# Kernel tuning notes

Hardware: AMD Instinct MI355X
Metric: run time of the kernel (lower is better)

## Reference

```python
import jax, jax.numpy as jnp
import numpy as np

N_WAY = 5
MAX_PER_CLASS = 256
SIGMA_GRID = np.array([0.5, 1.0, 2.0, 4.0], dtype=np.float32)
NUM_NEG = 1
GAMMA = 0.1
HARD_POOL = 8
MEDIAN_K = 512
EPS = 1e-12
LAMBDA_MMD = 0.1


def _pairwise_sq(x, y=None):
    # squared euclidean distances between rows of x [n,d] and y [m,d]
    if y is None:
        y = x
    x2 = jnp.sum(x * x, axis=1, keepdims=True)
    y2 = jnp.sum(y * y, axis=1, keepdims=True).T
    return jnp.maximum(x2 + y2 - 2.0 * (x @ y.T), 0.0)


def _row_norm(x):
    return x / (jnp.linalg.norm(x, axis=1, keepdims=True) + EPS)


def _rbf_multi(d, sigmas):
    # multi-bandwidth RBF kernel sum: sum_s exp(-d / (2 s^2))
    return jnp.sum(jnp.exp(-d[None] / (2.0 * sigmas[:, None, None] ** 2)), axis=0)


def _mmd2(Da, Db, Dab, sigmas):
    # biased MMD^2 estimator (unbiased=False)
    m = (_rbf_multi(Da, sigmas).mean() + _rbf_multi(Db, sigmas).mean()
         - 2.0 * _rbf_multi(Dab, sigmas).mean())
    return jnp.maximum(m, 0.0)


def _median_sigmas(xa, xb):
    # median-heuristic bandwidth (no grad); concat has <= MEDIAN_K rows by construction
    z = jnp.concatenate([xa, xb], axis=0)
    d = _pairwise_sq(z)
    ds = jnp.sort(d.ravel())
    n = ds.shape[0]
    nz = jnp.sum(d <= 0)  # number of zero entries (diag + exact dups)
    idx = jnp.minimum(nz + (n - nz - 1) // 2, n - 1)  # lower median of positive entries
    med = jnp.take(ds, idx)
    base = jnp.where(nz >= n, jnp.asarray(1.0, z.dtype), jnp.sqrt(med + 1e-6))
    return jax.lax.stop_gradient(base) * jnp.asarray(SIGMA_GRID, z.dtype)


def _gather_indices(l_s, l_q):
    # host-side ragged per-class index extraction + deterministic subsample
    ls = np.asarray(l_s)
    lq = np.asarray(l_q)
    sup, ns, qry, nq = {}, {}, {}, {}
    for c in range(1, N_WAY + 1):
        idx = np.nonzero(ls[c - 1] == 1)[0]
        if idx.size >= 2:
            ns[c] = int(idx.size)
            if idx.size > MAX_PER_CLASS:
                rng = np.random.default_rng(1000 + c)
                idx = idx[rng.permutation(idx.size)[:MAX_PER_CLASS]]
            sup[c] = idx
        m, nn = np.nonzero(lq == c)
        if m.size >= 2:
            nq[c] = int(m.size)
            if m.size > MAX_PER_CLASS:
                rng = np.random.default_rng(2000 + c)
                pick = rng.permutation(m.size)[:MAX_PER_CLASS]
                m, nn = m[pick], nn[pick]
            qry[c] = (m, nn)
    return sup, ns, qry, nq


def _class_feats(f_s, f_q, sup, qry):
    # gather per-class rows and L2-normalize them
    fq = jnp.transpose(f_q, (0, 2, 1))  # [M_B, Nb, C]
    xas = {c: _row_norm(f_s[c - 1].T[idx]) for c, idx in sup.items()}
    xbs = {c: _row_norm(fq[m, nn]) for c, (m, nn) in qry.items()}
    return xas, xbs


def _select_picks(f_s, f_q, sup, qry):
    # hard-negative selection on concrete values (detached in the original)
    xas, xbs = _class_feats(f_s, f_q, sup, qry)
    picks = {}
    for c in sorted(set(xas) & set(xbs)):
        xb = xbs[c]
        Db = _pairwise_sq(xb)
        sig_pos = _median_sigmas(xas[c], xb)
        neg = [k for k in xas if k != c]
        if NUM_NEG == 0 or not neg:
            picks[c] = []
            continue
        scr = [(float(_mmd2(_pairwise_sq(xas[k]), Db, _pairwise_sq(xas[k], xb), sig_pos)), k) for k in neg]
        scr.sort(key=lambda t: t[0])
        pool = [k for _, k in scr[:max(HARD_POOL, NUM_NEG)]]
        ex = [(float(_mmd2(_pairwise_sq(xas[k]), Db, _pairwise_sq(xas[k], xb), _median_sigmas(xas[k], xb))), k) for k in pool]
        ex.sort(key=lambda t: t[0])
        picks[c] = [k for _, k in ex[:NUM_NEG]]
    return picks


def _loss(f_s, f_q, sup, ns, qry, nq, picks):
    xas, xbs = _class_feats(f_s, f_q, sup, qry)
    total = jnp.zeros((), f_s.dtype)
    valid_w = jnp.zeros((), f_s.dtype)
    for c in sorted(set(xas) & set(xbs)):
        xa, xb = xas[c], xbs[c]
        Db = _pairwise_sq(xb)
        sig_pos = _median_sigmas(xa, xb)
        mmd_pos = _mmd2(_pairwise_sq(xa), Db, _pairwise_sq(xa, xb), sig_pos)
        negs = []
        for k in picks.get(c, []):
            xk = xas[k]
            sig_k = _median_sigmas(xk, xb)
            negs.append(_mmd2(_pairwise_sq(xk), Db, _pairwise_sq(xk, xb), sig_k))
        if negs:
            mmd_neg = jnp.stack(negs).mean()
            loss_c = jax.nn.relu(mmd_pos - mmd_neg + GAMMA)
        else:
            loss_c = mmd_pos
        w = (ns[c] * nq[c]) ** 0.5  # class_weight='sqrt_ns_nq'
        total = total + w * loss_c
        valid_w = valid_w + w
    return LAMBDA_MMD * total / jnp.maximum(valid_w, EPS)


def setup_inputs() -> dict:
    key = jax.random.key(0)
    k1, k2, k3, k4 = jax.random.split(key, 4)
    return {
        "f_s": jax.random.normal(k1, (5, 256, 16384), jnp.float32),
        "l_s": jax.random.randint(k2, (5, 16384), 0, 2, jnp.int32),
        "f_q": jax.random.normal(k3, (5, 256, 65536), jnp.float32),
        "l_q": jax.random.randint(k4, (5, 65536), 0, 6, jnp.int32),
    }


def reference(f_s, l_s, f_q, l_q):
    sup, ns, qry, nq = _gather_indices(l_s, l_q)
    picks = _select_picks(f_s, f_q, sup, qry)
    return _loss(f_s, f_q, sup, ns, qry, nq, picks)
```

## Files before the change

kernel.cpp:

```cpp
#include <hip/hip_runtime.h>

struct U128 { unsigned long long hi, lo; };

__device__ __forceinline__ U128 u128_mul(U128 a, U128 b) {
  U128 r;
  r.lo = a.lo * b.lo;
  r.hi = __umul64hi(a.lo, b.lo) + a.hi * b.lo + a.lo * b.hi;
  return r;
}
__device__ __forceinline__ U128 u128_add(U128 a, U128 b) {
  U128 r; r.lo = a.lo + b.lo; r.hi = a.hi + b.hi + (r.lo < a.lo ? 1ull : 0ull); return r;
}

struct Pcg64 {
  U128 state, inc;
};

__device__ __forceinline__ void pcg_step(Pcg64* r) {
  const U128 M = {0x2360ed051fc65da4ull, 0x4385df649fccf645ull};
  r->state = u128_add(u128_mul(r->state, M), r->inc);
}
__device__ __forceinline__ unsigned long long pcg_next64(Pcg64* r) {
  pcg_step(r);
  unsigned int rot = (unsigned int)(r->state.hi >> 58);
  unsigned long long x = r->state.hi ^ r->state.lo;
  return (x >> rot) | (x << ((64u - rot) & 63u));
}

__device__ __forceinline__ unsigned int ss_hashmix(unsigned int v, unsigned int* hc) {
  v ^= *hc; *hc = *hc * 0x931e8875u; v *= *hc; v ^= v >> 16; return v;
}
__device__ __forceinline__ unsigned int ss_mix(unsigned int x, unsigned int y) {
  unsigned int r = x * 0xca01f9ddu ^ y * 0x4973f715u; r ^= r >> 16; return r;
}
__device__ void pcg_seed(Pcg64* rng, unsigned int seed) {
  unsigned int pool[4]; unsigned int hc = 0x43b0d7e5u;
  pool[0] = ss_hashmix(seed, &hc);
  for (int i = 1; i < 4; ++i) pool[i] = ss_hashmix(0u, &hc);
  for (int s = 0; s < 4; ++s)
    for (int d = 0; d < 4; ++d)
      if (s != d) pool[d] = ss_mix(pool[d], ss_hashmix(pool[s], &hc));
  unsigned int hc2 = 0x8b51f9ddu;
  unsigned long long w64[4];
  for (int i = 0; i < 4; ++i) {
    unsigned int lo = pool[(2*i) & 3];
    lo ^= hc2; hc2 *= 0x58f38dedu; lo *= hc2; lo ^= lo >> 16;
    unsigned int hi = pool[(2*i+1) & 3];
    hi ^= hc2; hc2 *= 0x58f38dedu; hi *= hc2; hi ^= hi >> 16;
    w64[i] = (unsigned long long)lo | ((unsigned long long)hi << 32);
  }
  U128 initstate = {w64[0], w64[1]};
  U128 initseq   = {w64[2], w64[3]};
  rng->inc.hi = (initseq.hi << 1) | (initseq.lo >> 63);
  rng->inc.lo = (initseq.lo << 1) | 1ull;
  rng->state.hi = 0; rng->state.lo = 0;
  pcg_step(rng);
  rng->state = u128_add(rng->state, initstate);
  pcg_step(rng);
}

__device__ void pcg_advance(Pcg64* r, unsigned long long delta) {
  U128 acc_mult = {0ull, 1ull}, acc_plus = {0ull, 0ull};
  U128 cur_mult = {0x2360ed051fc65da4ull, 0x4385df649fccf645ull};
  U128 cur_plus = r->inc;
  while (delta) {
    if (delta & 1ull) {
      acc_mult = u128_mul(acc_mult, cur_mult);
      acc_plus = u128_add(u128_mul(acc_plus, cur_mult), cur_plus);
    }
    U128 one = {0ull, 1ull};
    U128 cm1 = u128_add(cur_mult, one);
    cur_plus = u128_mul(cm1, cur_plus);
    cur_mult = u128_mul(cur_mult, cur_mult);
    delta >>= 1;
  }
  r->state = u128_add(u128_mul(r->state, acc_mult), acc_plus);
}

#define S_LEN   16384
#define Q_LEN   65536
#define Q_TOT   327680
#define DFEAT   256
#define MAXS    256
#define CAPS64  24576
#define CAPQ64  98304
#define TILE    4096
#define STILES  (S_LEN / TILE)
#define QTILES  (Q_TOT / TILE)
#define NBLK_C  (5 * STILES + 5 * QTILES)
#define MSHARDS 8
#define MPASSES 8


__constant__ int c_kshift[MPASSES] = {27, 23, 19, 15, 11, 7, 3, 0};

__global__ __launch_bounds__(256) void k_draws(unsigned int* __restrict__ draws) {
  int t = blockIdx.x; int cls = t % 5; int isq = t / 5;
  unsigned int seed = (unsigned)(1000 + isq * 1000 + cls + 1);
  unsigned long long cap64 = isq ? CAPQ64 : CAPS64;
  unsigned int* dst = draws + (isq ? (10ull * CAPS64 + (unsigned long long)cls * 2 * CAPQ64)
                                   : ((unsigned long long)cls * 2 * CAPS64));
  Pcg64 rng; pcg_seed(&rng, seed);
  int tid = threadIdx.x;
  unsigned long long C = cap64 / 256ull;
  unsigned long long k0 = (unsigned long long)tid * C;
  pcg_advance(&rng, k0);
  uint2* d2 = (uint2*)dst;
  for (unsigned long long m = 0; m < C; ++m) {
    unsigned long long o = pcg_next64(&rng);
    d2[k0 + m] = make_uint2((unsigned int)o, (unsigned int)(o >> 32));
  }
}

__global__ __launch_bounds__(256) void k_count(const int* __restrict__ ls,
                                               const int* __restrict__ lq,
                                               int* __restrict__ cnts) {
  int b = blockIdx.x;
  const int* src; int matchval;
  if (b < 5 * STILES) {
    int cls = b / STILES, tl = b % STILES;
    src = ls + cls * S_LEN + tl * TILE; matchval = 1;
  } else {
    int bb = b - 5 * STILES; int cls = bb / QTILES, tl = bb % QTILES;
    src = lq + tl * TILE; matchval = cls + 1;
  }
  int tid = threadIdx.x;
  int cnt = 0;
  for (int k = 0; k < TILE; k += 256) cnt += (src[k + tid] == matchval) ? 1 : 0;
  __shared__ int red[256];
  red[tid] = cnt; __syncthreads();
  for (int s = 128; s > 0; s >>= 1) { if (tid < s) red[tid] += red[tid + s]; __syncthreads(); }
  if (tid == 0) cnts[b] = red[0];
}

__global__ void k_scan(const int* __restrict__ cnts, int* __restrict__ offs,
                       int* __restrict__ meta) {
  int t = threadIdx.x;
  if (t < 5) {
    int base = 0;
    for (int k = 0; k < STILES; ++k) {
      offs[t * STILES + k] = base; base += cnts[t * STILES + k];
    }
    meta[t] = base;
    meta[10 + t] = base < MAXS ? base : MAXS;
  } else if (t < 10) {
    int c = t - 5; int base = 0;
    for (int k = 0; k < QTILES; ++k) {
      int idx = 5 * STILES + c * QTILES + k;
      offs[idx] = base; base += cnts[idx];
    }
    meta[5 + c] = base;
    meta[15 + c] = base < MAXS ? base : MAXS;
  }
}

__global__ __launch_bounds__(256) void k_write(const int* __restrict__ ls,
                                               const int* __restrict__ lq,
                                               const int* __restrict__ offs,
                                               int* __restrict__ sup_list,
                                               int* __restrict__ qry_list) {
  int b = blockIdx.x;
  const int* src; int matchval; int* out; int ibase;
  if (b < 5 * STILES) {
    int cls = b / STILES, tl = b % STILES;
    src = ls + cls * S_LEN + tl * TILE; matchval = 1;
    out = sup_list + cls * S_LEN; ibase = tl * TILE;
  } else {
    int bb = b - 5 * STILES; int cls = bb / QTILES, tl = bb % QTILES;
    src = lq + tl * TILE; matchval = cls + 1;
    out = qry_list + (size_t)cls * Q_TOT; ibase = tl * TILE;
  }
  int tid = threadIdx.x; int w = tid >> 6, lane = tid & 63;
  unsigned long long lmask = (1ull << lane) - 1ull;
  __shared__ int wcnt[4];
  int base = offs[b];
  for (int k = 0; k < TILE; k += 256) {
    int i = k + tid;
    bool p = (src[i] == matchval);
    unsigned long long m = __ballot(p);
    if (lane == 0) wcnt[w] = __popcll(m);
    __syncthreads();
    int prev = 0;
    #pragma unroll
    for (int ww = 0; ww < 4; ++ww) prev += (ww < w) ? wcnt[ww] : 0;
    int tot = wcnt[0] + wcnt[1] + wcnt[2] + wcnt[3];
    if (p) out[base + prev + __popcll(m & lmask)] = ibase + i;
    __syncthreads();
    base += tot;
  }
}

__global__ __launch_bounds__(64) void k_consume(const int* __restrict__ meta,
                                                const unsigned int* __restrict__ draws,
                                                int* Jsup, int* Jqry) {
  int t = blockIdx.x; int cls = t % 5; int isq = t / 5;
  int n = meta[isq * 5 + cls];
  if (n <= MAXS) return;
  const unsigned int* d = draws + (isq ? (10ull * CAPS64 + (unsigned long long)cls * 2 * CAPQ64)
                                       : ((unsigned long long)cls * 2 * CAPS64));
  int* J = isq ? (Jqry + (size_t)cls * Q_TOT) : (Jsup + cls * S_LEN);
  int lane = threadIdx.x;
  unsigned long long lmask = (1ull << lane) - 1ull;
  unsigned long long lbit  = (1ull << lane);
  int i = n - 1;
  size_t p = 0;
  unsigned int v   = d[lane];
  unsigned int vn1 = d[64 + lane];
  unsigned int vn2 = d[128 + lane];
  unsigned int vn3 = d[192 + lane];
  for (;;) {
    unsigned int vfar = d[p + 256 + lane];
    unsigned long long rej = 0ull, acc = 0ull;
    for (;;) {
      unsigned long long unc = ~(rej | acc);
      int rbelow = __popcll(rej & lmask);
      int ubelow = __popcll(unc & lmask);
      int il_min = i - lane + rbelow;
      int il_max = il_min + ubelow;
      bool unres = (unc & lbit) != 0ull;
      unsigned int mlo = 0xFFFFFFFFu >> __clz(il_min);
      unsigned int mhi = 0xFFFFFFFFu >> __clz(il_max);
      unsigned int w = v & mlo;
      bool def_rej, hard;
      if (mlo == mhi) {
        def_rej = w > (unsigned int)il_max;
        hard = !def_rej && (w > (unsigned int)il_min);
      } else if (ubelow == 0) {
        def_rej = w > (unsigned int)il_min;
        hard = false;
      } else {
        def_rej = false;
        hard = true;
      }
      def_rej = def_rej && unres;
      hard = hard && unres;
      unsigned long long nr = __ballot(def_rej);
      unsigned long long hd = __ballot(hard);
      rej |= nr;
      acc |= unc & ~nr & ~hd;
      if (!hd) break;
    }
    int rbelow = __popcll(rej & lmask);
    int il = i - lane + rbelow;
    int totAcc = 64 - __popcll(rej);
    if ((acc & lbit) && il >= MAXS)
      J[il] = (int)(v & (0xFFFFFFFFu >> __clz(il)));
    int needed = i - (MAXS - 1);
    if (totAcc >= needed) break;
    i -= totAcc; p += 64;
    v = vn1; vn1 = vn2; vn2 = vn3; vn3 = vfar;
  }
}

__global__ __launch_bounds__(256) void k_hfill(const int* __restrict__ meta,
                                               const int* __restrict__ Jsup,
                                               const int* __restrict__ Jqry,
                                               unsigned int* __restrict__ Hsup,
                                               unsigned int* __restrict__ Hqry) {
  const int SB = 5 * (S_LEN / 256);
  int b = blockIdx.x;
  int cls, i; const int* J; unsigned int* H; int n;
  if (b < SB) {
    cls = b / (S_LEN / 256);
    i = (b % (S_LEN / 256)) * 256 + threadIdx.x;
    n = meta[cls];
    J = Jsup + cls * S_LEN; H = Hsup + cls * S_LEN;
  } else {
    b -= SB;
    cls = b / (Q_TOT / 256);
    i = (b % (Q_TOT / 256)) * 256 + threadIdx.x;
    n = meta[5 + cls];
    J = Jqry + (size_t)cls * Q_TOT; H = Hqry + (size_t)cls * Q_TOT;
  }
  if (i < MAXS || i >= n) return;
  int j = J[i];
  if (j != i) atomicMin(&H[j], (unsigned int)i);
}

__global__ __launch_bounds__(256) void k_chase(const int* __restrict__ meta,
                                               const int* __restrict__ sup_list,
                                               const int* __restrict__ qry_list,
                                               const unsigned int* __restrict__ Hsup,
                                               const unsigned int* __restrict__ Hqry,
                                               int* sel) {
  int t = blockIdx.x; int tid = threadIdx.x;
  int cls = t % 5; int isq = t / 5;
  int n = meta[isq * 5 + cls];
  const int* list; const unsigned int* H;
  if (!isq) { list = sup_list + cls * S_LEN; H = Hsup + cls * S_LEN; }
  else      { list = qry_list + (size_t)cls * Q_TOT; H = Hqry + (size_t)cls * Q_TOT; }
  int* s = sel + t * MAXS;
  if (n <= MAXS) { if (tid < n) s[tid] = list[tid]; return; }
  unsigned int v = (unsigned int)tid;
  unsigned int h = H[v];
  while (h != 0xFFFFFFFFu) { v = h; h = H[v]; }
  s[tid] = list[v];
}

__global__ __launch_bounds__(256) void k_gather(const float* __restrict__ f_s,
                                                const float* __restrict__ f_q,
                                                const int* __restrict__ meta,
                                                const int* __restrict__ sel,
                                                float* xa, float* xb) {
  int blk = blockIdx.x;
  int t = blk >> 3;
  int slab = blk & 7;
  int cls = t % 5; int isq = t / 5;
  int n = meta[10 + isq * 5 + cls];
  int tid = threadIdx.x;
  int row = slab * 32 + (tid >> 3);
  int dg = tid & 7;
  if (row >= n) return;
  int id = sel[t * MAXS + row];
  const float* src; size_t stride; float* dst;
  if (!isq) {
    src = f_s + (size_t)cls * DFEAT * S_LEN + id; stride = S_LEN;
    dst = xa + cls * (MAXS * DFEAT) + row * DFEAT;
  } else {
    int m = id >> 16; int nn = id & 0xFFFF;
    src = f_q + (size_t)m * DFEAT * Q_LEN + nn; stride = Q_LEN;
    dst = xb + cls * (MAXS * DFEAT) + row * DFEAT;
  }
  float v[32];
  #pragma unroll
  for (int dd = 0; dd < 32; ++dd)
    v[dd] = src[(size_t)(dg * 32 + dd) * stride];
  float ss = 0.f;
  #pragma unroll
  for (int dd = 0; dd < 32; ++dd) ss += v[dd] * v[dd];
  ss += __shfl_xor(ss, 1);
  ss += __shfl_xor(ss, 2);
  ss += __shfl_xor(ss, 4);
  float inv = 1.0f / (sqrtf(ss) + 1e-12f);
  #pragma unroll
  for (int dd = 0; dd < 32; ++dd) dst[dg * 32 + dd] = v[dd] * inv;
}

__global__ __launch_bounds__(256) void k_gram(const float* __restrict__ xa,
                                              const float* __restrict__ xb,
                                              float* Ga, float* Gb, float* Gab) {
  int b = blockIdx.x;
  int j = b >> 2; int tile = b & 3;
  int tr = (tile >> 1) * 128, tc = (tile & 1) * 128;
  const float *A, *B; float* G;
  if (j < 5)       { A = xa + j * 65536; B = A; G = Ga + j * 65536; }
  else if (j < 10) { int c = j - 5; A = xb + c * 65536; B = A; G = Gb + c * 65536; }
  else             { int p = j - 10; int k = p / 5, c = p % 5;
                     A = xa + k * 65536; B = xb + c * 65536; G = Gab + p * 65536; }
  __shared__ float As[128][33];
  __shared__ float Bs[128][33];
  int tid = threadIdx.x;
  int w = tid >> 6, lane = tid & 63;
  int wr = w >> 1, wc = w & 1;
  int lr = lane >> 3, lc = lane & 7;
  int orow = wr * 64 + lr * 8;
  int ocol = wc * 64 + lc * 8;
  float acc[8][8];
  #pragma unroll
  for (int r = 0; r < 8; ++r)
    #pragma unroll
    for (int s = 0; s < 8; ++s) acc[r][s] = 0.f;

  for (int k0 = 0; k0 < 256; k0 += 32) {
    #pragma unroll
    for (int e = 0; e < 4; ++e) {
      int idx = tid + e * 256;
      int row = idx >> 3;
      int c4  = idx & 7;
      float4 va = *(const float4*)(A + (size_t)(tr + row) * 256 + k0 + c4 * 4);
      As[row][c4 * 4 + 0] = va.x; As[row][c4 * 4 + 1] = va.y;
      As[row][c4 * 4 + 2] = va.z; As[row][c4 * 4 + 3] = va.w;
      float4 vb = *(const float4*)(B + (size_t)(tc + row) * 256 + k0 + c4 * 4);
      Bs[row][c4 * 4 + 0] = vb.x; Bs[row][c4 * 4 + 1] = vb.y;
      Bs[row][c4 * 4 + 2] = vb.z; Bs[row][c4 * 4 + 3] = vb.w;
    }
    __syncthreads();
    #pragma unroll 4
    for (int kk = 0; kk < 32; ++kk) {
      float a[8], bv[8];
      #pragma unroll
      for (int r = 0; r < 8; ++r) a[r] = As[orow + r][kk];
      #pragma unroll
      for (int s = 0; s < 8; ++s) bv[s] = Bs[ocol + s][kk];
      #pragma unroll
      for (int r = 0; r < 8; ++r)
        #pragma unroll
        for (int s = 0; s < 8; ++s) acc[r][s] += a[r] * bv[s];
    }
    __syncthreads();
  }
  #pragma unroll
  for (int r = 0; r < 8; ++r) {
    float* grow = G + (size_t)(tr + orow + r) * 256 + tc + ocol;
    *(float4*)(grow + 0) = make_float4(acc[r][0], acc[r][1], acc[r][2], acc[r][3]);
    *(float4*)(grow + 4) = make_float4(acc[r][4], acc[r][5], acc[r][6], acc[r][7]);
  }
}

__global__ __launch_bounds__(256) void k_diag(const float* __restrict__ Ga,
                                              const float* __restrict__ Gb,
                                              float* diagA, float* diagB) {
  int t = blockIdx.x; int i = threadIdx.x;
  if (t < 5) diagA[t * 256 + i] = Ga[t * 65536 + i * 257];
  else { int c = t - 5; diagB[c * 256 + i] = Gb[c * 65536 + i * 257]; }
}

__global__ __launch_bounds__(256) void k_conv(float* Ga, float* Gb, float* Gab,
                                              const float* __restrict__ diagA,
                                              const float* __restrict__ diagB) {
  int b = blockIdx.x; int j = b >> 3; int slab = b & 7; int tid = threadIdx.x;
  float* G; const float *dA, *dB;
  if (j < 5)       { G = Ga + j * 65536; dA = diagA + j * 256; dB = dA; }
  else if (j < 10) { int c = j - 5; G = Gb + c * 65536; dA = diagB + c * 256; dB = dA; }
  else             { int p = j - 10; int k = p / 5, c = p % 5;
                     G = Gab + p * 65536; dA = diagA + k * 256; dB = diagB + c * 256; }
  float db = dB[tid];
  for (int i = slab * 32; i < slab * 32 + 32; ++i) {
    float g = G[i * 256 + tid];
    float d = dA[i] + db - 2.0f * g;
    G[i * 256 + tid] = d > 0.f ? d : 0.f;
  }
}

__device__ __forceinline__ void med_select(const unsigned int* __restrict__ c,
                                           unsigned int lprev, unsigned int bprev,
                                           unsigned int r, int kprev,
                                           unsigned int* lo, unsigned int* base) {
  int j = 15;
  #pragma unroll
  for (int q = 14; q >= 0; --q)
    if (bprev + c[q] > r) j = q;
  *lo = lprev + ((unsigned int)j << kprev);
  *base = (j == 0) ? bprev : bprev + c[j - 1];
}

__global__ __launch_bounds__(256) void k_medpass(int t,
                                                 const int* __restrict__ meta,
                                                 const float* __restrict__ Da_all,
                                                 const float* __restrict__ Db_all,
                                                 const float* __restrict__ Dab_all,
                                                 unsigned int* __restrict__ bufAll,
                                                 unsigned int* __restrict__ loArr,
                                                 unsigned int* __restrict__ baseArr,
                                                 unsigned int* __restrict__ zcArr) {
  int b = blockIdx.x;
  int p = b / MSHARDS, sh = b % MSHARDS;
  int kcl = p / 5, ccl = p % 5;
  int tid = threadIdx.x;
  int nsf = meta[kcl], nqf = meta[5 + ccl];
  if (nsf < 2 || nqf < 2) return;
  int na = meta[10 + kcl], nb = meta[15 + ccl];
  const float4* A4 = (const float4*)(Da_all + kcl * 65536);
  const float4* B4 = (const float4*)(Db_all + ccl * 65536);
  const float4* C4 = (const float4*)(Dab_all + p * 65536);

  __shared__ unsigned int sh_lo[1], sh_base[1];
  __shared__ unsigned int wred[4][16];
  __shared__ unsigned int wzc[4];

  int ks = c_kshift[t];
  unsigned int N = (unsigned int)(na + nb) * (unsigned int)(na + nb);

  if (tid == 0) {
    unsigned int lo = 0, base = 0;
    if (t > 0) {
      unsigned int nz = zcArr[p];
      if (nz < N) {
        unsigned int r = nz + (N - nz - 1u) / 2u;
        unsigned int cprev[15];
        const unsigned int* cp = bufAll + ((size_t)(t - 1) * 25 + p) * 16;
        #pragma unroll
        for (int q = 0; q < 15; ++q) cprev[q] = cp[q];
        med_select(cprev, loArr[(t - 1) * 25 + p], baseArr[(t - 1) * 25 + p],
                   r, c_kshift[t - 1], &lo, &base);
      }
    }
    sh_lo[0] = lo; sh_base[0] = base;
    if (sh == 0) { loArr[t * 25 + p] = lo; baseArr[t * 25 + p] = base; }
  }
  __syncthreads();
  unsigned int lo = sh_lo[0];

  unsigned int cnt[15];
  #pragma unroll
  for (int j = 0; j < 15; ++j) cnt[j] = 0;
  unsigned int zc = 0;
  unsigned int span = 16u << ks;

  #define PROC_MAT(M4, nr, nc, W)                                             \
    for (int m = 0; m < 8; ++m) {                                             \
      int fidx = sh * 2048 + m * 256 + tid;                                   \
      float4 v = M4[fidx];                                                    \
      int row = fidx >> 6; int col0 = (fidx & 63) << 2;                       \
      unsigned int kb[4] = {__float_as_uint(v.x), __float_as_uint(v.y),       \
                            __float_as_uint(v.z), __float_as_uint(v.w)};      \
      _Pragma("unroll")                                                       \
      for (int cc = 0; cc < 4; ++cc) {                                        \
        bool valid = (row < (nr)) && (col0 + cc < (nc));                      \
        unsigned int key = kb[cc];                                            \
        if (t == 0) zc += (valid && key == 0u) ? (W) : 0u;                    \
        unsigned int d = key - lo;                                            \
        bool in = valid && (key >= lo) && (d < span);                         \
        _Pragma("unroll")                                                     \
        for (int j = 0; j < 15; ++j)                                          \
          cnt[j] += (in && d < ((unsigned int)(j + 1) << ks)) ? (W) : 0u;     \
      }                                                                       \
    }

  PROC_MAT(A4, na, na, 1u)
  PROC_MAT(B4, nb, nb, 1u)
  PROC_MAT(C4, na, nb, 2u)
  #undef PROC_MAT

  #pragma unroll
  for (int j = 0; j < 15; ++j)
    for (int o = 32; o > 0; o >>= 1) cnt[j] += __shfl_down(cnt[j], o);
  if (t == 0)
    for (int o = 32; o > 0; o >>= 1) zc += __shfl_down(zc, o);
  int w = tid >> 6, lane = tid & 63;
  if (lane == 0) {
    #pragma unroll
    for (int j = 0; j < 15; ++j) wred[w][j] = cnt[j];
    wzc[w] = zc;
  }
  __syncthreads();
  if (tid < 15) {
    unsigned int s = wred[0][tid] + wred[1][tid] + wred[2][tid] + wred[3][tid];
    atomicAdd(&bufAll[((size_t)t * 25 + p) * 16 + tid], s);
  }
  if (t == 0 && tid == 15) {
    unsigned int s = wzc[0] + wzc[1] + wzc[2] + wzc[3];
    atomicAdd(&zcArr[p], s);
  }
}

__global__ __launch_bounds__(256) void k_rbf(const int* __restrict__ meta,
                                             const float* __restrict__ Da_all,
                                             const float* __restrict__ Db_all,
                                             const float* __restrict__ Dab_all,
                                             const unsigned int* __restrict__ bufAll,
                                             const unsigned int* __restrict__ loArr,
                                             const unsigned int* __restrict__ baseArr,
                                             const unsigned int* __restrict__ zcArr,
                                             double* __restrict__ mmdsum) {
  int b = blockIdx.x;
  int p = b / MSHARDS, sh = b % MSHARDS;
  int kcl = p / 5, ccl = p % 5;
  int tid = threadIdx.x;
  int nsf = meta[kcl], nqf = meta[5 + ccl];
  if (nsf < 2 || nqf < 2) return;
  int na = meta[10 + kcl], nb = meta[15 + ccl];
  const float4* A4 = (const float4*)(Da_all + kcl * 65536);
  const float4* B4 = (const float4*)(Db_all + ccl * 65536);
  const float4* C4 = (const float4*)(Dab_all + p * 65536);

  unsigned int N = (unsigned int)(na + nb) * (unsigned int)(na + nb);
  unsigned int nz = zcArr[p];
  float base_s;
  if (nz >= N) base_s = 1.0f;
  else {
    unsigned int r = nz + (N - nz - 1u) / 2u;
    unsigned int cprev[15];
    const unsigned int* cp = bufAll + ((size_t)(MPASSES - 1) * 25 + p) * 16;
    #pragma unroll
    for (int q = 0; q < 15; ++q) cprev[q] = cp[q];
    unsigned int lo, bs;
    med_select(cprev, loArr[(MPASSES - 1) * 25 + p], baseArr[(MPASSES - 1) * 25 + p],
               r, 0, &lo, &bs);
    base_s = sqrtf(__uint_as_float(lo) + 1e-6f);
  }
  float g2 = base_s * base_s;
  float c0 = 1.0f / (2.0f * g2 * 0.25f);
  float c1 = 1.0f / (2.0f * g2 * 1.0f);
  float c2 = 1.0f / (2.0f * g2 * 4.0f);
  float c3 = 1.0f / (2.0f * g2 * 16.0f);

  double accA = 0.0, accB = 0.0, accAB = 0.0;
  #define RBF_MAT(M4, nr, nc, ACC)                                            \
    for (int m = 0; m < 8; ++m) {                                             \
      int fidx = sh * 2048 + m * 256 + tid;                                   \
      float4 v = M4[fidx];                                                    \
      int row = fidx >> 6; int col0 = (fidx & 63) << 2;                       \
      float vv[4] = {v.x, v.y, v.z, v.w};                                     \
      _Pragma("unroll")                                                       \
      for (int cc = 0; cc < 4; ++cc) {                                        \
        if ((row < (nr)) && (col0 + cc < (nc))) {                             \
          float d = vv[cc];                                                   \
          ACC += (double)(expf(-d * c0) + expf(-d * c1)                       \
                        + expf(-d * c2) + expf(-d * c3));                     \
        }                                                                     \
      }                                                                       \
    }
  RBF_MAT(A4, na, na, accA)
  RBF_MAT(B4, nb, nb, accB)
  RBF_MAT(C4, na, nb, accAB)
  #undef RBF_MAT

  for (int o = 32; o > 0; o >>= 1) {
    accA += __shfl_down(accA, o);
    accB += __shfl_down(accB, o);
    accAB += __shfl_down(accAB, o);
  }
  __shared__ double wsum[4][3];
  int w = tid >> 6, lane = tid & 63;
  if (lane == 0) { wsum[w][0] = accA; wsum[w][1] = accB; wsum[w][2] = accAB; }
  __syncthreads();
  if (tid == 0) {
    double sA = wsum[0][0] + wsum[1][0] + wsum[2][0] + wsum[3][0];
    double sB = wsum[0][1] + wsum[1][1] + wsum[2][1] + wsum[3][1];
    double sC = wsum[0][2] + wsum[1][2] + wsum[2][2] + wsum[3][2];
    atomicAdd(&mmdsum[p * 3 + 0], sA);
    atomicAdd(&mmdsum[p * 3 + 1], sB);
    atomicAdd(&mmdsum[p * 3 + 2], sC);
  }
}

__global__ void k_final(const int* __restrict__ meta, const double* __restrict__ mmdsum,
                        float* out) {
  if (threadIdx.x != 0 || blockIdx.x != 0) return;
  double total = 0.0, vw = 0.0;
  for (int c = 0; c < 5; ++c) {
    int nsf = meta[c], nqf = meta[5 + c];
    if (nsf < 2 || nqf < 2) continue;
    int nbq = meta[15 + c];
    double mm[5];
    for (int k = 0; k < 5; ++k) {
      if (meta[k] < 2) { mm[k] = 0.0; continue; }
      int naa = meta[10 + k];
      int pp = k * 5 + c;
      double meanA  = mmdsum[pp * 3 + 0] / ((double)naa * (double)naa);
      double meanB  = mmdsum[pp * 3 + 1] / ((double)nbq * (double)nbq);
      double meanAB = mmdsum[pp * 3 + 2] / ((double)naa * (double)nbq);
      double m = meanA + meanB - 2.0 * meanAB;
      mm[k] = m > 0.0 ? m : 0.0;
    }
    double pos = mm[c];
    bool any = false; double best = 0.0;
    for (int k = 0; k < 5; ++k) {
      if (k == c || meta[k] < 2) continue;
      if (!any || mm[k] < best) { best = mm[k]; any = true; }
    }
    double lc = any ? fmax(pos - best + 0.1, 0.0) : pos;
    double w = sqrt((double)nsf * (double)nqf);
    total += w * lc; vw += w;
  }
  out[0] = (float)(0.1 * total / fmax(vw, 1e-12));
}

extern "C" void kernel_launch(void* const* d_in, const int* in_sizes, int n_in,
                              void* d_out, int out_size, void* d_ws, size_t ws_size,
                              hipStream_t stream) {
  const float* f_s = (const float*)d_in[0];
  const int*   l_s = (const int*)d_in[1];
  const float* f_q = (const float*)d_in[2];
  const int*   l_q = (const int*)d_in[3];
  float* out = (float*)d_out;
  char* ws = (char*)d_ws;

  size_t off = 0;
  auto take = [&](size_t bytes) -> void* {
    void* p = ws + off;
    off = (off + bytes + 255) & ~(size_t)255;
    return p;
  };
  int*   meta     = (int*)take(32 * 4);
  int*   cnts     = (int*)take(NBLK_C * 4);
  int*   offs     = (int*)take(NBLK_C * 4);
  int*   sup_list = (int*)take((size_t)5 * S_LEN * 4);
  int*   qry_list = (int*)take((size_t)5 * Q_TOT * 4);
  int*   Jsup     = (int*)take((size_t)5 * S_LEN * 4);
  int*   Jqry     = (int*)take((size_t)5 * Q_TOT * 4);
  unsigned int* draws = (unsigned int*)take((10ull * CAPS64 + 10ull * CAPQ64) * 4);
  int*   sel      = (int*)take((size_t)10 * MAXS * 4);
  float* xa       = (float*)take((size_t)5 * 65536 * 4);
  float* xb       = (float*)take((size_t)5 * 65536 * 4);
  float* Ga       = (float*)take((size_t)5 * 65536 * 4);
  float* Gb       = (float*)take((size_t)5 * 65536 * 4);
  float* Gab      = (float*)take((size_t)25 * 65536 * 4);
  float* diagA    = (float*)take((size_t)5 * 256 * 4);
  float* diagB    = (float*)take((size_t)5 * 256 * 4);
  unsigned int* bufAll  = (unsigned int*)take((size_t)MPASSES * 25 * 16 * 4);
  unsigned int* loArr   = (unsigned int*)take((size_t)MPASSES * 25 * 4);
  unsigned int* baseArr = (unsigned int*)take((size_t)MPASSES * 25 * 4);
  unsigned int* zcArr   = (unsigned int*)take(25 * 4);
  double* mmdsum  = (double*)take(25 * 3 * 8);
  if (off > ws_size) return;

  unsigned int* Hsup = draws;
  unsigned int* Hqry = draws + (size_t)5 * S_LEN;
  size_t hbytes = ((size_t)5 * S_LEN + (size_t)5 * Q_TOT) * 4;

  k_draws<<<10, 256, 0, stream>>>(draws);
  k_count<<<NBLK_C, 256, 0, stream>>>(l_s, l_q, cnts);
  k_scan<<<1, 64, 0, stream>>>(cnts, offs, meta);
  k_write<<<NBLK_C, 256, 0, stream>>>(l_s, l_q, offs, sup_list, qry_list);
  k_consume<<<10, 64, 0, stream>>>(meta, draws, Jsup, Jqry);
  hipMemsetAsync(Hsup, 0xFF, hbytes, stream);
  {
    int nblk = 5 * (S_LEN / 256) + 5 * (Q_TOT / 256);
    k_hfill<<<nblk, 256, 0, stream>>>(meta, Jsup, Jqry, Hsup, Hqry);
  }
  k_chase<<<10, 256, 0, stream>>>(meta, sup_list, qry_list, Hsup, Hqry, sel);
  k_gather<<<80, 256, 0, stream>>>(f_s, f_q, meta, sel, xa, xb);
  k_gram<<<140, 256, 0, stream>>>(xa, xb, Ga, Gb, Gab);
  k_diag<<<10, 256, 0, stream>>>(Ga, Gb, diagA, diagB);
  k_conv<<<280, 256, 0, stream>>>(Ga, Gb, Gab, diagA, diagB);

  hipMemsetAsync(bufAll, 0, (size_t)MPASSES * 25 * 16 * 4, stream);
  hipMemsetAsync(zcArr, 0, 25 * 4, stream);
  hipMemsetAsync(mmdsum, 0, 25 * 3 * 8, stream);
  for (int t = 0; t < MPASSES; ++t)
    k_medpass<<<25 * MSHARDS, 256, 0, stream>>>(t, meta, Ga, Gb, Gab,
                                                bufAll, loArr, baseArr, zcArr);
  k_rbf<<<25 * MSHARDS, 256, 0, stream>>>(meta, Ga, Gb, Gab,
                                          bufAll, loArr, baseArr, zcArr, mmdsum);
  k_final<<<1, 64, 0, stream>>>(meta, mmdsum, out);
}
```

Baseline: 835.0 us.

## Widen bounded-random rejection consumer to 256 threads with LDS-staged coalesced output

After: 797.9 us. 4.4% less time.

```diff
diff --git a/kernel.cpp b/kernel.cpp
--- a/kernel.cpp
+++ b/kernel.cpp
@@ -190,43 +190,54 @@
   }
 }
 
-__global__ __launch_bounds__(64) void k_consume(const int* __restrict__ meta,
-                                                const unsigned int* __restrict__ draws,
-                                                int* Jsup, int* Jqry) {
+__global__ __launch_bounds__(256) void k_consume(const int* __restrict__ meta,
+                                                 const unsigned int* __restrict__ draws,
+                                                 int* Jsup, int* Jqry) {
+  __shared__ unsigned long long bal[2][4];
+  __shared__ unsigned int ring[8192];
   int t = blockIdx.x; int cls = t % 5; int isq = t / 5;
   int n = meta[isq * 5 + cls];
   if (n <= MAXS) return;
   const unsigned int* d = draws + (isq ? (10ull * CAPS64 + (unsigned long long)cls * 2 * CAPQ64)
                                        : ((unsigned long long)cls * 2 * CAPS64));
   int* J = isq ? (Jqry + (size_t)cls * Q_TOT) : (Jsup + cls * S_LEN);
-  int lane = threadIdx.x;
-  unsigned long long lmask = (1ull << lane) - 1ull;
-  unsigned long long lbit  = (1ull << lane);
+  int tid = threadIdx.x;
+  int w = tid >> 6, lane = tid & 63;
+  unsigned long long lbit = 1ull << lane;
+  unsigned long long lmask_w = lbit - 1ull;
   int i = n - 1;
   size_t p = 0;
-  unsigned int v   = d[lane];
-  unsigned int vn1 = d[64 + lane];
-  unsigned int vn2 = d[128 + lane];
-  unsigned int vn3 = d[192 + lane];
-  for (;;) {
-    unsigned int vfar = d[p + 256 + lane];
-    unsigned long long rej = 0ull, acc = 0ull;
+  int flushed = 0;
+  const int cap = n - MAXS;
+
+  auto step256 = [&](unsigned int v) -> bool {
+    unsigned long long r0 = 0, r1 = 0, r2 = 0, r3 = 0;
+    unsigned long long a0 = 0, a1 = 0, a2 = 0, a3 = 0;
     for (;;) {
-      unsigned long long unc = ~(rej | acc);
-      int rbelow = __popcll(rej & lmask);
-      int ubelow = __popcll(unc & lmask);
-      int il_min = i - lane + rbelow;
-      int il_max = il_min + ubelow;
-      bool unres = (unc & lbit) != 0ull;
+      unsigned long long u0 = ~(r0 | a0), u1 = ~(r1 | a1);
+      unsigned long long u2 = ~(r2 | a2), u3 = ~(r3 | a3);
+      unsigned long long myR = (w == 0) ? r0 : (w == 1) ? r1 : (w == 2) ? r2 : r3;
+      unsigned long long myU = (w == 0) ? u0 : (w == 1) ? u1 : (w == 2) ? u2 : u3;
+      int rb = __popcll(myR & lmask_w)
+             + ((w > 0) ? __popcll(r0) : 0)
+             + ((w > 1) ? __popcll(r1) : 0)
+             + ((w > 2) ? __popcll(r2) : 0);
+      int ub = __popcll(myU & lmask_w)
+             + ((w > 0) ? __popcll(u0) : 0)
+             + ((w > 1) ? __popcll(u1) : 0)
+             + ((w > 2) ? __popcll(u2) : 0);
+      bool unres = (myU & lbit) != 0ull;
+      int il_min = i - tid + rb;
+      int il_max = il_min + ub;
       unsigned int mlo = 0xFFFFFFFFu >> __clz(il_min);
       unsigned int mhi = 0xFFFFFFFFu >> __clz(il_max);
-      unsigned int w = v & mlo;
+      unsigned int wv = v & mlo;
       bool def_rej, hard;
       if (mlo == mhi) {
-        def_rej = w > (unsigned int)il_max;
-        hard = !def_rej && (w > (unsigned int)il_min);
-      } else if (ubelow == 0) {
-        def_rej = w > (unsigned int)il_min;
+        def_rej = wv > (unsigned int)il_max;
+        hard = !def_rej && (wv > (unsigned int)il_min);
+      } else if (ub == 0) {
+        def_rej = wv > (unsigned int)il_min;
         hard = false;
       } else {
         def_rej = false;
@@ -234,22 +245,66 @@
       }
       def_rej = def_rej && unres;
       hard = hard && unres;
-      unsigned long long nr = __ballot(def_rej);
-      unsigned long long hd = __ballot(hard);
-      rej |= nr;
-      acc |= unc & ~nr & ~hd;
-      if (!hd) break;
-    }
-    int rbelow = __popcll(rej & lmask);
-    int il = i - lane + rbelow;
-    int totAcc = 64 - __popcll(rej);
-    if ((acc & lbit) && il >= MAXS)
-      J[il] = (int)(v & (0xFFFFFFFFu >> __clz(il)));
+      unsigned long long wnr = __ballot(def_rej);
+      unsigned long long whd = __ballot(hard);
+      if (lane == 0) { bal[0][w] = wnr; bal[1][w] = whd; }
+      __syncthreads();
+      unsigned long long n0 = bal[0][0], n1 = bal[0][1], n2 = bal[0][2], n3 = bal[0][3];
+      unsigned long long h0 = bal[1][0], h1 = bal[1][1], h2 = bal[1][2], h3 = bal[1][3];
+      __syncthreads();
+      r0 |= n0; r1 |= n1; r2 |= n2; r3 |= n3;
+      a0 |= u0 & ~n0 & ~h0; a1 |= u1 & ~n1 & ~h1;
+      a2 |= u2 & ~n2 & ~h2; a3 |= u3 & ~n3 & ~h3;
+      if (!(h0 | h1 | h2 | h3)) break;
+    }
+    unsigned long long myR = (w == 0) ? r0 : (w == 1) ? r1 : (w == 2) ? r2 : r3;
+    unsigned long long myA = (w == 0) ? a0 : (w == 1) ? a1 : (w == 2) ? a2 : a3;
+    int rbf = __popcll(myR & lmask_w)
+            + ((w > 0) ? __popcll(r0) : 0)
+            + ((w > 1) ? __popcll(r1) : 0)
+            + ((w > 2) ? __popcll(r2) : 0);
+    int il = i - tid + rbf;
+    int totAcc = 256 - (__popcll(r0) + __popcll(r1) + __popcll(r2) + __popcll(r3));
+    if ((myA & lbit) && il >= MAXS) {
+      int g = (n - 1) - il;
+      ring[g & 8191] = v & (0xFFFFFFFFu >> __clz(il));
+    }
     int needed = i - (MAXS - 1);
-    if (totAcc >= needed) break;
-    i -= totAcc; p += 64;
-    v = vn1; vn1 = vn2; vn2 = vn3; vn3 = vfar;
-  }
+    if (totAcc >= needed) return true;
+    i -= totAcc;
+    return false;
+  };
+
+  unsigned int v0 = d[tid],        v1 = d[256 + tid];
+  unsigned int v2 = d[512 + tid],  v3 = d[768 + tid];
+  for (;;) {
+    unsigned int nv0 = d[p + 1024 + tid];
+    unsigned int nv1 = d[p + 1280 + tid];
+    unsigned int nv2 = d[p + 1536 + tid];
+    unsigned int nv3 = d[p + 1792 + tid];
+    bool done;
+    if      (step256(v0)) done = true;
+    else if (step256(v1)) done = true;
+    else if (step256(v2)) done = true;
+    else if (step256(v3)) done = true;
+    else done = false;
+    if (done) break;
+    int avail = (n - 1) - i; if (avail > cap) avail = cap;
+    while (avail - flushed >= 4096) {
+      __syncthreads();
+      #pragma unroll
+      for (int k = 0; k < 16; ++k) {
+        int g = flushed + k * 256 + tid;
+        J[(n - 1) - g] = (int)ring[g & 8191];
+      }
+      flushed += 4096;
+    }
+    p += 1024;
+    v0 = nv0; v1 = nv1; v2 = nv2; v3 = nv3;
+  }
+  __syncthreads();
+  for (int g = flushed + tid; g < cap; g += 256)
+    J[(n - 1) - g] = (int)ring[g & 8191];
 }
 
 __global__ __launch_bounds__(256) void k_hfill(const int* __restrict__ meta,
@@ -694,7 +749,7 @@
   k_count<<<NBLK_C, 256, 0, stream>>>(l_s, l_q, cnts);
   k_scan<<<1, 64, 0, stream>>>(cnts, offs, meta);
   k_write<<<NBLK_C, 256, 0, stream>>>(l_s, l_q, offs, sup_list, qry_list);
-  k_consume<<<10, 64, 0, stream>>>(meta, draws, Jsup, Jqry);
+  k_consume<<<10, 256, 0, stream>>>(meta, draws, Jsup, Jqry);
   hipMemsetAsync(Hsup, 0xFF, hbytes, stream);
   {
     int nblk = 5 * (S_LEN / 256) + 5 * (Q_TOT / 256);
```
